# Optimization experiments

Hardware: AMD Instinct MI355X
Metric: run time of the kernel (lower is better)

Reference implementation:

```python
import jax, jax.numpy as jnp
import numpy as np

B, S, E, H = 4, 2048, 1024, 16
D = E // H  # per-head dim = 64


def setup_inputs() -> dict:
    key = jax.random.key(0)
    k1, k2, k3 = jax.random.split(key, 3)
    x = jax.random.normal(k1, (B, S, E), dtype=jnp.float32)
    # per-head nn.Linear(d, 3d, bias=False) weights, torch layout [3d, d]
    W_qkv = jax.random.normal(k2, (H, 3 * D, D), dtype=jnp.float32) * (D ** -0.5)
    # output projection nn.Linear(E, E, bias=False), torch layout [E, E]
    W_out = jax.random.normal(k3, (E, E), dtype=jnp.float32) * (E ** -0.5)
    return {"x": x, "W_qkv": W_qkv, "W_out": W_out}


def reference(x, W_qkv, W_out):
    b, s, e = x.shape
    h, td, d = W_qkv.shape  # td = 3*d
    # chunk along embedding dim -> [b, s, h, d]
    xh = x.reshape(b, s, h, d)
    # per-head linear: y = x @ W.T ; qkv layout from torch view(..., 3, d):
    # first d outputs are q, next d are k, last d are v
    qkv = jnp.einsum('bshd,hed->bshe', xh, W_qkv)  # [b, s, h, 3d]
    qkv = qkv.reshape(b, s, h, 3, d)
    q = qkv[..., 0, :].transpose(0, 2, 1, 3)  # [b, h, s, d]
    k = qkv[..., 1, :].transpose(0, 2, 1, 3)
    v = qkv[..., 2, :].transpose(0, 2, 1, 3)
    scores = jnp.einsum('bhid,bhjd->bhij', q, k) * (d ** -0.5)
    attn = jax.nn.softmax(scores, axis=-1)
    out = jnp.einsum('bhij,bhjd->bhid', attn, v)  # [b, h, s, d]
    out = out.transpose(0, 2, 1, 3).reshape(b, s, e)
    return out @ W_out.T
```

## Files before the change

### kernel.cpp

```cpp
#include <hip/hip_runtime.h>
#include <hip/hip_bf16.h>

#define NBATCH 4
#define NS 2048
#define NE 1024
#define NH 16
#define ND 64

typedef __attribute__((ext_vector_type(4))) float f32x4;
typedef __attribute__((ext_vector_type(16))) float f32x16;
typedef __attribute__((ext_vector_type(8))) short s16x8;
typedef __attribute__((ext_vector_type(2))) unsigned u32x2;

__device__ __forceinline__ unsigned short f2bf(float f) {
  union { float f; unsigned u; } v; v.f = f;
  return (unsigned short)((v.u + 0x7fffu + ((v.u >> 16) & 1u)) >> 16);
}

__device__ __forceinline__ unsigned cvt_pk_bf16(float lo, float hi) {
  unsigned r;
  asm("v_cvt_pk_bf16_f32 %0, %1, %2" : "=v"(r) : "v"(lo), "v"(hi));
  return r;
}

typedef const __attribute__((address_space(1))) void* gas_t;
typedef __attribute__((address_space(3))) void* las_t;

__global__ __launch_bounds__(256) void cvt_kernel(
    const float* __restrict__ wqkv, const float* __restrict__ wout,
    unsigned short* __restrict__ wqb, unsigned short* __restrict__ wob) {
  const int NQ = NH * 3 * ND * ND / 4, NO = NE * NE / 4;
  const int total = NQ + NO;
  for (int i = blockIdx.x * blockDim.x + threadIdx.x; i < total;
       i += gridDim.x * blockDim.x) {
    const float4* s; unsigned short* d; int j;
    if (i < NQ) { s = (const float4*)wqkv; d = wqb; j = i; }
    else        { s = (const float4*)wout; d = wob; j = i - NQ; }
    float4 v = s[j];
    ushort4 o;
    o.x = f2bf(v.x); o.y = f2bf(v.y); o.z = f2bf(v.z); o.w = f2bf(v.w);
    ((ushort4*)d)[j] = o;
  }
}

__global__ __launch_bounds__(256) void qkv_kernel(
    const float* __restrict__ x, const unsigned short* __restrict__ wqb,
    unsigned short* __restrict__ Qb, unsigned short* __restrict__ Kb,
    unsigned short* __restrict__ Vt) {
  __shared__ __align__(16) unsigned short wlds[192 * 64];
  int blk = blockIdx.x;
  int st = blk & 31;
  int bh = blk >> 5;
  int h = bh & 15;
  int b = bh >> 4;
  int tid = threadIdx.x, w = tid >> 6, l = tid & 63, lm = l & 15, lg = l >> 4;
  int s0 = st * 64 + w * 16;

  {
    const unsigned short* wg_ = wqb + h * 3 * ND * ND;
    int r8 = l >> 3;
    int chg = (l & 7) ^ r8;
#pragma unroll
    for (int i = 0; i < 6; i++) {
      int row = i * 32 + w * 8;
      __builtin_amdgcn_global_load_lds(
          (gas_t)(wg_ + (size_t)(row + r8) * ND + chg * 8),
          (las_t)(wlds + row * ND), 16, 0, 0);
    }
  }

  const float* xrow = x + (size_t)(b * NS + s0 + lm) * NE + h * ND;
  float4 f0 = *(const float4*)(xrow + lg * 8);
  float4 f1 = *(const float4*)(xrow + lg * 8 + 4);
  float4 f2 = *(const float4*)(xrow + 32 + lg * 8);
  float4 f3 = *(const float4*)(xrow + 32 + lg * 8 + 4);
  union { unsigned u[4]; s16x8 v; } A0, A1;
  A0.u[0] = cvt_pk_bf16(f0.x, f0.y); A0.u[1] = cvt_pk_bf16(f0.z, f0.w);
  A0.u[2] = cvt_pk_bf16(f1.x, f1.y); A0.u[3] = cvt_pk_bf16(f1.z, f1.w);
  A1.u[0] = cvt_pk_bf16(f2.x, f2.y); A1.u[1] = cvt_pk_bf16(f2.z, f2.w);
  A1.u[2] = cvt_pk_bf16(f3.x, f3.y); A1.u[3] = cvt_pk_bf16(f3.z, f3.w);
  s16x8 a0 = A0.v, a1 = A1.v;

  __syncthreads();

  const char* wl = (const char*)wlds;
  int baseA = lm * 128 + ((lg ^ (lm & 7)) * 16);
  int baseB = lm * 128 + (((4 + lg) ^ (lm & 7)) * 16);

  size_t bhS = (size_t)bh * NS;
  const float QSCALE = 0.125f * 1.44269504089f;

#pragma unroll
  for (int nb = 0; nb < 12; nb++) {
    s16x8 w0 = *(const s16x8*)(wl + nb * 2048 + baseA);
    s16x8 w1 = *(const s16x8*)(wl + nb * 2048 + baseB);
    f32x4 acc = (f32x4){0.f, 0.f, 0.f, 0.f};
    acc = __builtin_amdgcn_mfma_f32_16x16x32_bf16(a0, w0, acc, 0, 0, 0);
    acc = __builtin_amdgcn_mfma_f32_16x16x32_bf16(a1, w1, acc, 0, 0, 0);
    int e = nb * 16 + lm;
    if (nb < 4) {
#pragma unroll
      for (int r = 0; r < 4; r++)
        Qb[(bhS + s0 + lg * 4 + r) * ND + e] = f2bf(acc[r] * QSCALE);
    } else if (nb < 8) {
#pragma unroll
      for (int r = 0; r < 4; r++)
        Kb[(bhS + s0 + lg * 4 + r) * ND + (e - 64)] = f2bf(acc[r]);
    } else {
#pragma unroll
      for (int r = 0; r < 4; r++)
        Vt[((size_t)bh * ND + (e - 128)) * NS + s0 + lg * 4 + r] = f2bf(acc[r]);
    }
  }
}


#define STAGE_TO(BUFP)                                                         \
  {                                                                            \
    unsigned short* lp = (BUFP) + w * 2048;                                    \
    _Pragma("unroll")                                                          \
    for (int i = 0; i < 4; i++)                                                \
      __builtin_amdgcn_global_load_lds((gas_t)(gsrc + i * istep),              \
                                       (las_t)(lp + i * 512), 16, 0, 0);       \
    gsrc += gstep;                                                             \
  }

#define COMPUTE(BUFBASE)                                                       \
  {                                                                            \
    const char* kb_ = (const char*)(BUFBASE);                                  \
    s16x8 k0[4], k1[4];                                                        \
    _Pragma("unroll")                                                          \
    for (int dk = 0; dk < 4; dk++) {                                           \
      k0[dk] = *(const s16x8*)(kb_ + off0[dk]);                                \
      k1[dk] = *(const s16x8*)(kb_ + off0[dk] + 4096);                         \
    }                                                                          \
    f32x16 s0, s1;                                                             \
    s0 = __builtin_amdgcn_mfma_f32_32x32x16_bf16(k0[0], qf[0], zero16, 0, 0, 0);\
    s1 = __builtin_amdgcn_mfma_f32_32x32x16_bf16(k1[0], qf[0], zero16, 0, 0, 0);\
    _Pragma("unroll")                                                          \
    for (int dk = 1; dk < 4; dk++) {                                           \
      s0 = __builtin_amdgcn_mfma_f32_32x32x16_bf16(k0[dk], qf[dk], s0, 0, 0, 0);\
      s1 = __builtin_amdgcn_mfma_f32_32x32x16_bf16(k1[dk], qf[dk], s1, 0, 0, 0);\
    }                                                                          \
    s16x8 vf0[4], vf1[4];                                                      \
    _Pragma("unroll")                                                          \
    for (int ks = 0; ks < 4; ks++) {                                           \
      vf0[ks] = *(const s16x8*)(kb_ + off0[ks] + 8192);                        \
      vf1[ks] = *(const s16x8*)(kb_ + off0[ks] + 12288);                       \
    }                                                                          \
    _Pragma("unroll")                                                          \
    for (int r = 0; r < 16; r++) {                                             \
      s0[r] = __builtin_amdgcn_exp2f(s0[r]);                                   \
      s1[r] = __builtin_amdgcn_exp2f(s1[r]);                                   \
    }                                                                          \
           \
    s16x8 pa[4];                                                               \
    _Pragma("unroll")                                                          \
    for (int ks = 0; ks < 4; ks++) {                                           \
      const f32x16& pt = (ks >= 2) ? s1 : s0;                                  \
      const int R = (ks & 1) * 8;                                              \
      unsigned a0 = cvt_pk_bf16(pt[R + 0], pt[R + 1]);                         \
      unsigned a1 = cvt_pk_bf16(pt[R + 2], pt[R + 3]);                         \
      unsigned b0 = cvt_pk_bf16(pt[R + 4], pt[R + 5]);                         \
      unsigned b1 = cvt_pk_bf16(pt[R + 6], pt[R + 7]);                         \
      u32x2 r0 = __builtin_amdgcn_permlane32_swap(a0, b0, false, false);       \
      u32x2 r1 = __builtin_amdgcn_permlane32_swap(a1, b1, false, false);       \
      union { unsigned u[4]; s16x8 v; } fr;                                    \
      fr.u[0] = r0[0]; fr.u[1] = r1[0]; fr.u[2] = r0[1]; fr.u[3] = r1[1];      \
      pa[ks] = fr.v;                                                           \
    }                                                                          \
                                       \
    _Pragma("unroll")                                                          \
    for (int ks = 0; ks < 4; ks++) {                                           \
      o0 = __builtin_amdgcn_mfma_f32_32x32x16_bf16(vf0[ks], pa[ks], o0, 0, 0, 0);\
      o1 = __builtin_amdgcn_mfma_f32_32x32x16_bf16(vf1[ks], pa[ks], o1, 0, 0, 0);\
      accl = __builtin_amdgcn_mfma_f32_32x32x16_bf16(ones, pa[ks], accl, 0, 0, 0);\
    }                                                                          \
  }

__global__ __launch_bounds__(256) void attn_kernel(
    const unsigned short* __restrict__ Qb, const unsigned short* __restrict__ Kb,
    const unsigned short* __restrict__ Vt, unsigned short* __restrict__ AOb) {
  __shared__ __align__(16) unsigned short smem[24576];
  int blk = blockIdx.x;
  int wg = (blk & 7) * 128 + (blk >> 3);
  int qt = wg & 15;
  int bh = wg >> 4;
  int h = bh & 15;
  int b = bh >> 4;
  int tid = threadIdx.x, w = tid >> 6, l = tid & 63, c = l & 31, hi = l >> 5;
  int q0 = qt * 128 + w * 32;

  const unsigned short* Qh = Qb + (size_t)bh * NS * ND;
  const unsigned short* Kh = Kb + (size_t)bh * NS * ND;
  const unsigned short* Vh = Vt + (size_t)bh * ND * NS;

  int lrow = (w & 1) * 32 + (l >> 3);
  int chg = (l & 7) ^ (l >> 3);
  const unsigned short* gsrc;
  size_t istep, gstep;
  if (w < 2) { gsrc = Kh + (size_t)lrow * ND + chg * 8;  istep = 8 * ND;   gstep = 64 * ND; }
  else       { gsrc = Vh + (size_t)lrow * NS + chg * 8;  istep = 8 * NS;   gstep = 64; }

  int off0[4];
#pragma unroll
  for (int dk = 0; dk < 4; dk++)
    off0[dk] = c * 128 + (((dk * 2 + hi) ^ (c & 7)) * 16);

  s16x8 qf[4];
#pragma unroll
  for (int dk = 0; dk < 4; dk++)
    qf[dk] = *(const s16x8*)(Qh + (size_t)(q0 + c) * ND + dk * 16 + hi * 8);

  union { unsigned u[4]; s16x8 v; } onesu;
  onesu.u[0] = onesu.u[1] = onesu.u[2] = onesu.u[3] = 0x3F803F80u;
  s16x8 ones = onesu.v;

  f32x16 o0, o1, accl, zero16;
#pragma unroll
  for (int r = 0; r < 16; r++) { o0[r] = 0.f; o1[r] = 0.f; accl[r] = 0.f; zero16[r] = 0.f; }

  unsigned short* cA = smem;
  unsigned short* cB = smem + 8192;
  unsigned short* cC = smem + 16384;

  STAGE_TO(cA);
  STAGE_TO(cB);

  for (int t = 0; t < 31; t++) {
    asm volatile("s_waitcnt vmcnt(4)" ::: "memory");
    __builtin_amdgcn_s_barrier();
    if (t < 30) STAGE_TO(cC);
    COMPUTE(cA);
    unsigned short* tmp = cA; cA = cB; cB = cC; cC = tmp;
  }
  asm volatile("s_waitcnt vmcnt(0)" ::: "memory");
  __builtin_amdgcn_s_barrier();
  COMPUTE(cA);
  __builtin_amdgcn_s_barrier();

  float inv = 1.0f / accl[0];
  unsigned short* pl = smem + w * 2176;
#pragma unroll
  for (int dt = 0; dt < 2; dt++) {
#pragma unroll
    for (int rg = 0; rg < 4; rg++) {
      float v0 = (dt ? o1[rg * 4 + 0] : o0[rg * 4 + 0]) * inv;
      float v1 = (dt ? o1[rg * 4 + 1] : o0[rg * 4 + 1]) * inv;
      float v2 = (dt ? o1[rg * 4 + 2] : o0[rg * 4 + 2]) * inv;
      float v3 = (dt ? o1[rg * 4 + 3] : o0[rg * 4 + 3]) * inv;
      uint2 val;
      val.x = cvt_pk_bf16(v0, v1);
      val.y = cvt_pk_bf16(v2, v3);
      int dbase = dt * 32 + rg * 8 + 4 * hi;
      *reinterpret_cast<uint2*>(pl + c * 68 + dbase) = val;
    }
  }
  asm volatile("s_waitcnt lgkmcnt(0)" ::: "memory");
#pragma unroll
  for (int p = 0; p < 4; p++) {
    int row = p * 8 + (l >> 3);
    int co = (l & 7) * 8;
    uint2 x0 = *reinterpret_cast<const uint2*>(pl + row * 68 + co);
    uint2 x1 = *reinterpret_cast<const uint2*>(pl + row * 68 + co + 4);
    uint4 val; val.x = x0.x; val.y = x0.y; val.z = x1.x; val.w = x1.y;
    *reinterpret_cast<uint4*>(AOb + ((size_t)(b * NS + q0 + row)) * NE + h * ND + co) = val;
  }
}


#define STAGEP(BUF, koff)                                                      \
  {                                                                            \
    unsigned short* la = &smem[(BUF)][w * 512];                                \
    unsigned short* lb = &smem[(BUF)][8192 + w * 512];                         \
    _Pragma("unroll")                                                          \
    for (int i = 0; i < 2; i++) {                                              \
      __builtin_amdgcn_global_load_lds((gas_t)(gA + (size_t)i * 64 * NE + (koff)),\
                                       (las_t)(la + i * 4096), 16, 0, 0);      \
      __builtin_amdgcn_global_load_lds((gas_t)(gB + (size_t)i * 64 * NE + (koff)),\
                                       (las_t)(lb + i * 4096), 16, 0, 0);      \
    }                                                                          \
  }

__global__ __launch_bounds__(512) void proj_kernel(
    const unsigned short* __restrict__ A, const unsigned short* __restrict__ Bw,
    float* __restrict__ C) {
  __shared__ __align__(16) unsigned short smem[2][16384];
  int blk = blockIdx.x;
  int xcd = blk & 7, idx = blk >> 3;
  int bm = xcd * 8 + (idx >> 3);
  int bn = idx & 7;
  int tid = threadIdx.x, w = tid >> 6, l = tid & 63, c = l & 31, hi = l >> 5;
  int wr = w >> 2, wc = w & 3;
  int m0 = bm * 128, n0 = bn * 128;

  int srow = tid >> 3;
  int g = (tid & 7) ^ ((tid >> 3) & 7);
  const unsigned short* gA = A + (size_t)(m0 + srow) * NE + g * 8;
  const unsigned short* gB = Bw + (size_t)(n0 + srow) * NE + g * 8;

  int offA[2][4], offB[4];
#pragma unroll
  for (int mt = 0; mt < 2; mt++)
#pragma unroll
    for (int ks = 0; ks < 4; ks++)
      offA[mt][ks] = (wr * 64 + mt * 32 + c) * 128 + (((ks * 2 + hi) ^ (c & 7)) * 16);
#pragma unroll
  for (int ks = 0; ks < 4; ks++)
    offB[ks] = (wc * 32 + c) * 128 + (((ks * 2 + hi) ^ (c & 7)) * 16);

  f32x16 a0, a1;
#pragma unroll
  for (int r = 0; r < 16; r++) { a0[r] = 0.f; a1[r] = 0.f; }

  STAGEP(0, 0);
  __syncthreads();

  int cur = 0;
  for (int t = 0; t < 16; t++) {
    if (t < 15) STAGEP(cur ^ 1, (t + 1) * 64);
    {
      const char* ab = (const char*)&smem[cur][0];
      const char* bb = (const char*)&smem[cur][8192];
#pragma unroll
      for (int ks = 0; ks < 4; ks++) {
        s16x8 fa0 = *(const s16x8*)(ab + offA[0][ks]);
        s16x8 fa1 = *(const s16x8*)(ab + offA[1][ks]);
        s16x8 fb  = *(const s16x8*)(bb + offB[ks]);
        a0 = __builtin_amdgcn_mfma_f32_32x32x16_bf16(fa0, fb, a0, 0, 0, 0);
        a1 = __builtin_amdgcn_mfma_f32_32x32x16_bf16(fa1, fb, a1, 0, 0, 0);
      }
    }
    __syncthreads();
    cur ^= 1;
  }

#pragma unroll
  for (int mt = 0; mt < 2; mt++) {
    const f32x16& acc = mt == 0 ? a0 : a1;
#pragma unroll
    for (int r = 0; r < 16; r++) {
      int mrow = m0 + wr * 64 + mt * 32 + (r & 3) + 8 * (r >> 2) + 4 * hi;
      int ncol = n0 + wc * 32 + c;
      C[(size_t)mrow * NE + ncol] = acc[r];
    }
  }
}

extern "C" void kernel_launch(void* const* d_in, const int* in_sizes, int n_in,
                              void* d_out, int out_size, void* d_ws, size_t ws_size,
                              hipStream_t stream) {
  const float* x    = (const float*)d_in[0];
  const float* wqkv = (const float*)d_in[1];
  const float* wout = (const float*)d_in[2];
  float* out = (float*)d_out;
  char* ws = (char*)d_ws;

  size_t off = 0;
  unsigned short* wqb = (unsigned short*)(ws + off); off += (size_t)NH * 3 * ND * ND * 2;
  unsigned short* wob = (unsigned short*)(ws + off); off += (size_t)NE * NE * 2;
  unsigned short* Qb  = (unsigned short*)(ws + off); off += (size_t)NBATCH * NH * NS * ND * 2;
  unsigned short* Kb  = (unsigned short*)(ws + off); off += (size_t)NBATCH * NH * NS * ND * 2;
  unsigned short* Vt  = (unsigned short*)(ws + off); off += (size_t)NBATCH * NH * NS * ND * 2;
  unsigned short* AOb = (unsigned short*)(ws + off); off += (size_t)NBATCH * NS * NE * 2;

  cvt_kernel<<<1024, 256, 0, stream>>>(wqkv, wout, wqb, wob);
  qkv_kernel<<<2048, 256, 0, stream>>>(x, wqb, Qb, Kb, Vt);
  attn_kernel<<<1024, 256, 0, stream>>>(Qb, Kb, Vt, AOb);
  proj_kernel<<<512, 512, 0, stream>>>(AOb, wob, out);
}
```

Before: 133.5 us.

## Retile output projection GEMM to 256x128 blocks with 64x64 per-wave tiles

New measurement: 133.4 us. Within noise of the previous version (-0.0%).

```diff
diff --git a/kernel.cpp b/kernel.cpp
--- a/kernel.cpp
+++ b/kernel.cpp
@@ -114,7 +114,6 @@
   }
 }
 
-
 #define STAGE_TO(BUFP)                                                         \
   {                                                                            \
     unsigned short* lp = (BUFP) + w * 2048;                                    \
@@ -153,7 +152,6 @@
       s0[r] = __builtin_amdgcn_exp2f(s0[r]);                                   \
       s1[r] = __builtin_amdgcn_exp2f(s1[r]);                                   \
     }                                                                          \
-           \
     s16x8 pa[4];                                                               \
     _Pragma("unroll")                                                          \
     for (int ks = 0; ks < 4; ks++) {                                           \
@@ -169,7 +167,6 @@
       fr.u[0] = r0[0]; fr.u[1] = r1[0]; fr.u[2] = r0[1]; fr.u[3] = r1[1];      \
       pa[ks] = fr.v;                                                           \
     }                                                                          \
-                                       \
     _Pragma("unroll")                                                          \
     for (int ks = 0; ks < 4; ks++) {                                           \
       o0 = __builtin_amdgcn_mfma_f32_32x32x16_bf16(vf0[ks], pa[ks], o0, 0, 0, 0);\
@@ -271,80 +268,97 @@
 
 #define STAGEP(BUF, koff)                                                      \
   {                                                                            \
-    unsigned short* la = &smem[(BUF)][w * 512];                                \
-    unsigned short* lb = &smem[(BUF)][8192 + w * 512];                         \
-    _Pragma("unroll")                                                          \
-    for (int i = 0; i < 2; i++) {                                              \
+    unsigned short* lbase = &smem[(BUF)][w * 512];                             \
+    _Pragma("unroll")                                                          \
+    for (int i = 0; i < 4; i++)                                                \
       __builtin_amdgcn_global_load_lds((gas_t)(gA + (size_t)i * 64 * NE + (koff)),\
-                                       (las_t)(la + i * 4096), 16, 0, 0);      \
-      __builtin_amdgcn_global_load_lds((gas_t)(gB + (size_t)i * 64 * NE + (koff)),\
-                                       (las_t)(lb + i * 4096), 16, 0, 0);      \
-    }                                                                          \
+                                       (las_t)(lbase + i * 4096), 16, 0, 0);   \
+    _Pragma("unroll")                                                          \
+    for (int j = 0; j < 2; j++)                                                \
+      __builtin_amdgcn_global_load_lds((gas_t)(gB + (size_t)j * 64 * NE + (koff)),\
+                                       (las_t)(lbase + 16384 + j * 4096, 16, 0, 0) ? 0 : 0, 16, 0, 0); \
+  }
+
+#undef STAGEP
+#define STAGEP(BUF, koff)                                                      \
+  {                                                                            \
+    unsigned short* lbase = &smem[(BUF)][w * 512];                             \
+    _Pragma("unroll")                                                          \
+    for (int i = 0; i < 4; i++)                                                \
+      __builtin_amdgcn_global_load_lds((gas_t)(gA + (size_t)i * 64 * NE + (koff)),\
+                                       (las_t)(lbase + i * 4096), 16, 0, 0);   \
+    _Pragma("unroll")                                                          \
+    for (int j = 0; j < 2; j++)                                                \
+      __builtin_amdgcn_global_load_lds((gas_t)(gB + (size_t)j * 64 * NE + (koff)),\
+                                       (las_t)(lbase + 16384 + j * 4096), 16, 0, 0); \
   }
 
 __global__ __launch_bounds__(512) void proj_kernel(
     const unsigned short* __restrict__ A, const unsigned short* __restrict__ Bw,
     float* __restrict__ C) {
-  __shared__ __align__(16) unsigned short smem[2][16384];
+  __shared__ __align__(16) unsigned short smem[2][24576];
   int blk = blockIdx.x;
-  int xcd = blk & 7, idx = blk >> 3;
-  int bm = xcd * 8 + (idx >> 3);
-  int bn = idx & 7;
+  int wg = (blk & 7) * 32 + (blk >> 3);
+  int bm = wg >> 3;
+  int bn = wg & 7;
   int tid = threadIdx.x, w = tid >> 6, l = tid & 63, c = l & 31, hi = l >> 5;
-  int wr = w >> 2, wc = w & 3;
-  int m0 = bm * 128, n0 = bn * 128;
+  int wr = w >> 1, wc = w & 1;
+  int m0 = bm * 256, n0 = bn * 128;
 
   int srow = tid >> 3;
-  int g = (tid & 7) ^ ((tid >> 3) & 7);
+  int g = (tid & 7) ^ (srow & 7);
   const unsigned short* gA = A + (size_t)(m0 + srow) * NE + g * 8;
   const unsigned short* gB = Bw + (size_t)(n0 + srow) * NE + g * 8;
 
-  int offA[2][4], offB[4];
+  int offA[2][4], offB[2][4];
 #pragma unroll
   for (int mt = 0; mt < 2; mt++)
 #pragma unroll
-    for (int ks = 0; ks < 4; ks++)
+    for (int ks = 0; ks < 4; ks++) {
       offA[mt][ks] = (wr * 64 + mt * 32 + c) * 128 + (((ks * 2 + hi) ^ (c & 7)) * 16);
-#pragma unroll
-  for (int ks = 0; ks < 4; ks++)
-    offB[ks] = (wc * 32 + c) * 128 + (((ks * 2 + hi) ^ (c & 7)) * 16);
-
-  f32x16 a0, a1;
-#pragma unroll
-  for (int r = 0; r < 16; r++) { a0[r] = 0.f; a1[r] = 0.f; }
+      offB[mt][ks] = 32768 + (wc * 64 + mt * 32 + c) * 128 + (((ks * 2 + hi) ^ (c & 7)) * 16);
+    }
+
+  f32x16 a00, a01, a10, a11;
+#pragma unroll
+  for (int r = 0; r < 16; r++) { a00[r] = 0.f; a01[r] = 0.f; a10[r] = 0.f; a11[r] = 0.f; }
 
   STAGEP(0, 0);
-  __syncthreads();
 
   int cur = 0;
   for (int t = 0; t < 16; t++) {
+    asm volatile("s_waitcnt vmcnt(0)" ::: "memory");
+    __builtin_amdgcn_s_barrier();
     if (t < 15) STAGEP(cur ^ 1, (t + 1) * 64);
     {
-      const char* ab = (const char*)&smem[cur][0];
-      const char* bb = (const char*)&smem[cur][8192];
+      const char* bb = (const char*)&smem[cur][0];
 #pragma unroll
       for (int ks = 0; ks < 4; ks++) {
-        s16x8 fa0 = *(const s16x8*)(ab + offA[0][ks]);
-        s16x8 fa1 = *(const s16x8*)(ab + offA[1][ks]);
-        s16x8 fb  = *(const s16x8*)(bb + offB[ks]);
-        a0 = __builtin_amdgcn_mfma_f32_32x32x16_bf16(fa0, fb, a0, 0, 0, 0);
-        a1 = __builtin_amdgcn_mfma_f32_32x32x16_bf16(fa1, fb, a1, 0, 0, 0);
+        s16x8 fa0 = *(const s16x8*)(bb + offA[0][ks]);
+        s16x8 fa1 = *(const s16x8*)(bb + offA[1][ks]);
+        s16x8 fb0 = *(const s16x8*)(bb + offB[0][ks]);
+        s16x8 fb1 = *(const s16x8*)(bb + offB[1][ks]);
+        a00 = __builtin_amdgcn_mfma_f32_32x32x16_bf16(fa0, fb0, a00, 0, 0, 0);
+        a01 = __builtin_amdgcn_mfma_f32_32x32x16_bf16(fa0, fb1, a01, 0, 0, 0);
+        a10 = __builtin_amdgcn_mfma_f32_32x32x16_bf16(fa1, fb0, a10, 0, 0, 0);
+        a11 = __builtin_amdgcn_mfma_f32_32x32x16_bf16(fa1, fb1, a11, 0, 0, 0);
       }
     }
-    __syncthreads();
     cur ^= 1;
   }
 
 #pragma unroll
-  for (int mt = 0; mt < 2; mt++) {
-    const f32x16& acc = mt == 0 ? a0 : a1;
-#pragma unroll
-    for (int r = 0; r < 16; r++) {
-      int mrow = m0 + wr * 64 + mt * 32 + (r & 3) + 8 * (r >> 2) + 4 * hi;
-      int ncol = n0 + wc * 32 + c;
-      C[(size_t)mrow * NE + ncol] = acc[r];
-    }
-  }
+  for (int mt = 0; mt < 2; mt++)
+#pragma unroll
+    for (int nt = 0; nt < 2; nt++) {
+      const f32x16& acc = mt == 0 ? (nt == 0 ? a00 : a01) : (nt == 0 ? a10 : a11);
+#pragma unroll
+      for (int r = 0; r < 16; r++) {
+        int mrow = m0 + wr * 64 + mt * 32 + (r & 3) + 8 * (r >> 2) + 4 * hi;
+        int ncol = n0 + wc * 64 + nt * 32 + c;
+        C[(size_t)mrow * NE + ncol] = acc[r];
+      }
+    }
 }
 
 extern "C" void kernel_launch(void* const* d_in, const int* in_sizes, int n_in,
@@ -367,5 +381,5 @@
   cvt_kernel<<<1024, 256, 0, stream>>>(wqkv, wout, wqb, wob);
   qkv_kernel<<<2048, 256, 0, stream>>>(x, wqb, Qb, Kb, Vt);
   attn_kernel<<<1024, 256, 0, stream>>>(Qb, Kb, Vt, AOb);
-  proj_kernel<<<512, 512, 0, stream>>>(AOb, wob, out);
-}
+  proj_kernel<<<256, 512, 0, stream>>>(AOb, wob, out);
+}
```
